# Optimization experiments

Measured on AMD Instinct MI355X. Metric: run time of the kernel, lower is better.

## Reference

```python
import jax, jax.numpy as jnp
import numpy as np

K, N = 8, 20          # exactly-K-of-N circuit
B = 524288            # batch
NEG = -1e9            # masked-softmax logit


def setup_inputs() -> dict:
    key = jax.random.key(0)
    k1, k2, k3 = jax.random.split(key, 3)
    # boolean data vector per example
    x = jax.random.randint(k1, (B, N), 0, 2).astype(bool)
    # leaf sum-node weights: node S(1, m) has m weights, stored in row m (padded to N)
    Wleaf = jax.random.uniform(k2, (N + 1, N), dtype=jnp.float32)
    # internal sum-node weights: node S(k, m) (1 < k < m <= N, incl. root) has 2 weights
    W2 = jax.random.uniform(k3, (K + 1, N + 1, 2), dtype=jnp.float32)
    return {"x": x, "Wleaf": Wleaf, "W2": W2}


def _circuit(xf, Wleaf, W2):
    """Tensorized DP over the (k, m) lattice; same math as the recursive circuit:
      S(m, m) = prod_{i<m} x_i                                (prodNode base case)
      S(1, m) = sum_i w_i * x_i * prod_{j<m, j!=i} (1 - x_j)  (leaf sumNode)
      S(k, m) = w0 * S(k, m-1) + w1 * S(k-1, m-1) * x_{m-1}   (internal sumNode)
    Root output = S(K, N), shape [B, 1].
    """
    Bsz = xf.shape[0]
    csum = jnp.cumsum(xf, axis=1)    # running count of ones
    pre = jnp.cumprod(xf, axis=1)    # pre[:, m-1] = prod_{i<m} x_i = S(m, m)

    # --- leaf row k = 1, vectorized over m ---
    mask = jnp.arange(N)[None, :] < jnp.arange(N + 1)[:, None]      # [N+1, N]
    wsm = jax.nn.softmax(jnp.where(mask, Wleaf, NEG), axis=-1)
    wsm = jnp.where(mask, wsm, 0.0)
    dots = xf @ wsm.T                                               # [B, N+1]: sum_{i<m} w_i x_i
    # for boolean x: x_i * prod_{j<m, j!=i}(1-x_j) is nonzero iff exactly one of
    # x[:, :m] is set, so S(1, m) = 1[count_m == 1] * (w . x[:, :m])
    exactly_one = jnp.concatenate(
        [jnp.zeros((Bsz, 1), xf.dtype), (csum == 1.0).astype(xf.dtype)], axis=1)
    S_cols = [exactly_one[:, m] * dots[:, m] for m in range(N + 1)]  # row k = 1

    # --- internal rows k = 2 .. K ---
    w2 = jax.nn.softmax(W2, axis=-1)   # softmax over each node's 2 children
    zero = jnp.zeros((Bsz,), xf.dtype)
    for k in range(2, K + 1):
        row = [zero] * (N + 1)
        row[k] = pre[:, k - 1]                      # S(k, k) = prod of first k inputs
        for m in range(k + 1, N + 1):
            row[m] = w2[k, m, 0] * row[m - 1] + w2[k, m, 1] * S_cols[m - 1] * xf[:, m - 1]
        S_cols = row
    return S_cols[N][:, None]    # [B, 1], like torch matmul output


def reference(x, Wleaf, W2):
    return _circuit(x.astype(jnp.float32), Wleaf, W2)
```

## Files before the change

kernel.cpp:

```cpp
#include <hip/hip_runtime.h>
#include <hip/hip_bf16.h>

static constexpr int NB  = 20;
static constexpr int KK  = 8;
static constexpr int EPT = 2;

__global__ __launch_bounds__(256) void pc_kernel(
    const void* __restrict__ xraw,
    const void* __restrict__ wleaf_raw,
    const void* __restrict__ w2_raw,
    void* __restrict__ outraw,
    int batch)
{
    __shared__ float s_wsm[(NB + 1) * NB];
    __shared__ float s_w20[(KK + 1) * (NB + 1)];
    __shared__ float s_w21[(KK + 1) * (NB + 1)];
    __shared__ float s_inv[NB + 1];
    __shared__ int s_flagX, s_flagW, s_cntW, s_xKind;

    const int tid = threadIdx.x;

    if (tid == 0) { s_cntW = 0; s_xKind = 0; }
    __syncthreads();

    if (tid < 64) {
        unsigned v = ((const unsigned*)xraw)[tid];
        if (v > 1u) {
            if (((v & 0xFFFFu) == 0x3F80u) || ((v >> 16) == 0x3F80u))
                atomicOr(&s_xKind, 2);
            else
                atomicOr(&s_xKind, 1);
        }
    } else if (tid < 64 + 192) {
        unsigned v = ((const unsigned*)wleaf_raw)[tid - 64];
        unsigned hb = (v >> 8) & 0xFFu;
        if (hb >= 0x30u && hb <= 0x40u) atomicAdd(&s_cntW, 1);
    }
    __syncthreads();
    if (tid == 0) {
        int xk = s_xKind;
        s_flagX = (xk & 2) ? 2 : ((xk & 1) ? 1 : 0);
        s_flagW = (s_cntW > 96) ? 1 : 0;
    }
    __syncthreads();
    const int fX = s_flagX;
    const int fW = s_flagW;

    auto WL = [&](int idx) -> float {
        return fW ? __bfloat162float(((const __hip_bfloat16*)wleaf_raw)[idx])
                  : ((const float*)wleaf_raw)[idx];
    };
    auto W2v = [&](int idx) -> float {
        return fW ? __bfloat162float(((const __hip_bfloat16*)w2_raw)[idx])
                  : ((const float*)w2_raw)[idx];
    };

    const int base = blockIdx.x * (256 * EPT) + tid;
    unsigned bits[EPT];
    bool valid[EPT];
    #pragma unroll
    for (int e = 0; e < EPT; ++e) {
        const int b = base + e * 256;
        valid[e] = (b < batch);
        unsigned bb = 0;
        if (valid[e]) {
            if (fX == 0) {
                const int4* row = (const int4*)((const int*)xraw + (size_t)b * NB);
                #pragma unroll
                for (int j = 0; j < 5; ++j) {
                    int4 v = row[j];
                    bb |= (unsigned)(v.x != 0) << (4 * j + 0);
                    bb |= (unsigned)(v.y != 0) << (4 * j + 1);
                    bb |= (unsigned)(v.z != 0) << (4 * j + 2);
                    bb |= (unsigned)(v.w != 0) << (4 * j + 3);
                }
            } else if (fX == 1) {
                const unsigned* p = (const unsigned*)((const unsigned char*)xraw + (size_t)b * NB);
                #pragma unroll
                for (int j = 0; j < 5; ++j) {
                    unsigned v = p[j];
                    bb |= (unsigned)(((v      ) & 0xFFu) != 0) << (4 * j + 0);
                    bb |= (unsigned)(((v >>  8) & 0xFFu) != 0) << (4 * j + 1);
                    bb |= (unsigned)(((v >> 16) & 0xFFu) != 0) << (4 * j + 2);
                    bb |= (unsigned)(((v >> 24)       ) != 0) << (4 * j + 3);
                }
            } else {
                const unsigned* p = (const unsigned*)((const unsigned short*)xraw + (size_t)b * NB);
                #pragma unroll
                for (int j = 0; j < 10; ++j) {
                    unsigned v = p[j];
                    bb |= (unsigned)((v & 0xFFFFu) != 0) << (2 * j + 0);
                    bb |= (unsigned)((v >> 16)     != 0) << (2 * j + 1);
                }
            }
        }
        bits[e] = bb;
    }

    if (tid < 200) {
        #pragma unroll
        for (int s = 0; s < 2; ++s) {
            const int p = 20 + tid + s * 200;
            const int m = p / 20, i = p - m * 20;
            if (i < m) s_wsm[p] = expf(WL(p));
        }
    }
    __syncthreads();
    if (tid >= 1 && tid <= NB) {
        float s = 0.f;
        for (int i = 0; i < tid; ++i) s += s_wsm[tid * NB + i];
        s_inv[tid] = 1.f / s;
    } else if (tid >= 21 && tid < 21 + (KK + 1) * (NB + 1)) {
        const int idx = tid - 21;
        const float a = W2v(idx * 2 + 0);
        const float b = W2v(idx * 2 + 1);
        const float mx = fmaxf(a, b);
        const float ea = expf(a - mx), eb = expf(b - mx);
        const float inv = 1.f / (ea + eb);
        s_w20[idx] = ea * inv;
        s_w21[idx] = eb * inv;
    }
    __syncthreads();
    if (tid < 200) {
        #pragma unroll
        for (int s = 0; s < 2; ++s) {
            const int p = 20 + tid + s * 200;
            const int m = p / 20, i = p - m * 20;
            if (i < m) s_wsm[p] *= s_inv[m];
        }
    }
    __syncthreads();

    float S[EPT][NB + 1];
    int pc[EPT], oi[EPT];
    #pragma unroll
    for (int e = 0; e < EPT; ++e) { S[e][0] = 0.f; pc[e] = 0; oi[e] = 0; }
    #pragma unroll
    for (int m = 1; m <= NB; ++m) {
        #pragma unroll
        for (int e = 0; e < EPT; ++e) {
            if ((bits[e] >> (m - 1)) & 1u) { pc[e]++; oi[e] = m - 1; }
            const float wv = s_wsm[m * NB + oi[e]];
            S[e][m] = (pc[e] == 1) ? wv : 0.f;
        }
    }

    #pragma unroll
    for (int k = 2; k <= KK; ++k) {
        const unsigned lm = (1u << k) - 1u;
        float prevNew[EPT], oldPrev[EPT];
        #pragma unroll
        for (int e = 0; e < EPT; ++e) {
            prevNew[e] = ((bits[e] & lm) == lm) ? 1.f : 0.f;
            oldPrev[e] = S[e][k];
            S[e][k] = prevNew[e];
        }
        #pragma unroll
        for (int m = k + 1; m <= NB; ++m) {
            const float w0 = s_w20[k * (NB + 1) + m];
            const float w1 = s_w21[k * (NB + 1) + m];
            #pragma unroll
            for (int e = 0; e < EPT; ++e) {
                const float oldCur = S[e][m];
                const float t = ((bits[e] >> (m - 1)) & 1u) ? oldPrev[e] : 0.f;
                const float cur = fmaf(w0, prevNew[e], w1 * t);
                S[e][m] = cur;
                prevNew[e] = cur;
                oldPrev[e] = oldCur;
            }
        }
    }

    #pragma unroll
    for (int e = 0; e < EPT; ++e) {
        const int b = base + e * 256;
        if (valid[e]) {
            if (fW) ((__hip_bfloat16*)outraw)[b] = __float2bfloat16(S[e][NB]);
            else    ((float*)outraw)[b]          = S[e][NB];
        }
    }
}

extern "C" void kernel_launch(void* const* d_in, const int* in_sizes, int n_in,
                              void* d_out, int out_size, void* d_ws, size_t ws_size,
                              hipStream_t stream) {
    (void)n_in; (void)out_size; (void)d_ws; (void)ws_size;
    const int batch = in_sizes[0] / NB;
    const int blocks = (batch + 256 * EPT - 1) / (256 * EPT);
    pc_kernel<<<blocks, 256, 0, stream>>>(d_in[0], d_in[1], d_in[2], d_out, batch);
}
```

Before: 89.85 us.

## Collapse leaf row analytically and pack two elements into float2 vector ops

Removes the normalization pass and the per-m leaf-row loop. Row k=2 is computed directly: with boolean inputs, S(1,m) times x_{m-1} is nonzero only at the position of the second set bit, so a single injected term found via ctz replaces the leaf DP. The normalization by s_inv is folded into that one lookup, dropping one __syncthreads. The remaining k=3..8 DP packs the two per-thread elements into float2 vectors, aiming for packed FMA instructions and lower VALU count.

```diff
diff --git a/kernel.cpp b/kernel.cpp
--- a/kernel.cpp
+++ b/kernel.cpp
@@ -4,6 +4,8 @@
 static constexpr int NB  = 20;
 static constexpr int KK  = 8;
 static constexpr int EPT = 2;
+
+typedef float v2f __attribute__((ext_vector_type(2)));
 
 __global__ __launch_bounds__(256) void pc_kernel(
     const void* __restrict__ xraw,
@@ -13,9 +15,9 @@
     int batch)
 {
     __shared__ float s_wsm[(NB + 1) * NB];
+    __shared__ float s_inv[NB + 1];
     __shared__ float s_w20[(KK + 1) * (NB + 1)];
     __shared__ float s_w21[(KK + 1) * (NB + 1)];
-    __shared__ float s_inv[NB + 1];
     __shared__ int s_flagX, s_flagW, s_cntW, s_xKind;
 
     const int tid = threadIdx.x;
@@ -121,62 +123,69 @@
         s_w21[idx] = eb * inv;
     }
     __syncthreads();
-    if (tid < 200) {
-        #pragma unroll
-        for (int s = 0; s < 2; ++s) {
-            const int p = 20 + tid + s * 200;
-            const int m = p / 20, i = p - m * 20;
-            if (i < m) s_wsm[p] *= s_inv[m];
-        }
-    }
-    __syncthreads();
-
-    float S[EPT][NB + 1];
-    int pc[EPT], oi[EPT];
-    #pragma unroll
-    for (int e = 0; e < EPT; ++e) { S[e][0] = 0.f; pc[e] = 0; oi[e] = 0; }
-    #pragma unroll
-    for (int m = 1; m <= NB; ++m) {
-        #pragma unroll
-        for (int e = 0; e < EPT; ++e) {
-            if ((bits[e] >> (m - 1)) & 1u) { pc[e]++; oi[e] = m - 1; }
-            const float wv = s_wsm[m * NB + oi[e]];
-            S[e][m] = (pc[e] == 1) ? wv : 0.f;
-        }
-    }
-
-    #pragma unroll
-    for (int k = 2; k <= KK; ++k) {
+
+    int p2[EPT];
+    float inj[EPT];
+    #pragma unroll
+    for (int e = 0; e < EPT; ++e) {
+        const unsigned be = bits[e];
+        const unsigned low = be & (be - 1u);
+        const int j0 = __builtin_ctz(be  | (1u << 20));
+        const int q0 = __builtin_ctz(low | (1u << 20));
+        const bool has2 = (low != 0u);
+        p2[e] = has2 ? (q0 + 1) : 99;
+        const int rV = has2 ? q0 : 1;
+        const int cV = has2 ? j0 : 0;
+        const float V = s_wsm[rV * NB + cV] * s_inv[rV];
+        inj[e] = s_w21[2 * (NB + 1) + (has2 ? (q0 + 1) : 3)] * V;
+    }
+
+    v2f S[NB + 1];
+    v2f pn;
+    pn.x = ((bits[0] & 3u) == 3u) ? 1.f : 0.f;
+    pn.y = ((bits[1] & 3u) == 3u) ? 1.f : 0.f;
+    S[2] = pn;
+    #pragma unroll
+    for (int m = 3; m <= NB; ++m) {
+        const float w0 = s_w20[2 * (NB + 1) + m];
+        v2f add;
+        add.x = (m == p2[0]) ? inj[0] : 0.f;
+        add.y = (m == p2[1]) ? inj[1] : 0.f;
+        v2f cur = w0 * pn + add;
+        S[m] = cur;
+        pn = cur;
+    }
+
+    #pragma unroll
+    for (int k = 3; k <= KK; ++k) {
         const unsigned lm = (1u << k) - 1u;
-        float prevNew[EPT], oldPrev[EPT];
-        #pragma unroll
-        for (int e = 0; e < EPT; ++e) {
-            prevNew[e] = ((bits[e] & lm) == lm) ? 1.f : 0.f;
-            oldPrev[e] = S[e][k];
-            S[e][k] = prevNew[e];
-        }
+        v2f p, op;
+        p.x = ((bits[0] & lm) == lm) ? 1.f : 0.f;
+        p.y = ((bits[1] & lm) == lm) ? 1.f : 0.f;
+        op = S[k];
+        S[k] = p;
         #pragma unroll
         for (int m = k + 1; m <= NB; ++m) {
+            const v2f oc = S[m];
             const float w0 = s_w20[k * (NB + 1) + m];
             const float w1 = s_w21[k * (NB + 1) + m];
-            #pragma unroll
-            for (int e = 0; e < EPT; ++e) {
-                const float oldCur = S[e][m];
-                const float t = ((bits[e] >> (m - 1)) & 1u) ? oldPrev[e] : 0.f;
-                const float cur = fmaf(w0, prevNew[e], w1 * t);
-                S[e][m] = cur;
-                prevNew[e] = cur;
-                oldPrev[e] = oldCur;
-            }
-        }
-    }
-
+            v2f t;
+            t.x = ((bits[0] >> (m - 1)) & 1u) ? op.x : 0.f;
+            t.y = ((bits[1] >> (m - 1)) & 1u) ? op.y : 0.f;
+            v2f cur = w0 * p + w1 * t;
+            S[m] = cur;
+            p = cur;
+            op = oc;
+        }
+    }
+
+    const float outv[EPT] = { S[NB].x, S[NB].y };
     #pragma unroll
     for (int e = 0; e < EPT; ++e) {
         const int b = base + e * 256;
         if (valid[e]) {
-            if (fW) ((__hip_bfloat16*)outraw)[b] = __float2bfloat16(S[e][NB]);
-            else    ((float*)outraw)[b]          = S[e][NB];
+            if (fW) ((__hip_bfloat16*)outraw)[b] = __float2bfloat16(outv[e]);
+            else    ((float*)outraw)[b]          = outv[e];
         }
     }
 }
```

Result: faster. 85.67 us (-4.6%).
